# Performance work log

Measured on AMD Instinct MI355X. Metric: run time of the kernel, lower is better.

Reference implementation:

```python
import jax, jax.numpy as jnp
import numpy as np

EMBED_DIM = 1024
NUM_HEADS = 16
HEAD_DIM = EMBED_DIM // NUM_HEADS
LN_EPS = 1e-12
B, S = 2, 2048


def setup_inputs() -> dict:
    key = jax.random.key(0)
    ks = jax.random.split(key, 12)
    scale = 1.0 / np.sqrt(EMBED_DIM)
    d = EMBED_DIM
    return {
        "in_features": jax.random.normal(ks[0], (B, S, d), dtype=jnp.float32),
        "tgt_mask": jnp.ones((B, S), dtype=jnp.float32),
        "Wq": jax.random.normal(ks[1], (d, d), dtype=jnp.float32) * scale,
        "bq": jnp.zeros((d,), dtype=jnp.float32),
        "Wk": jax.random.normal(ks[2], (d, d), dtype=jnp.float32) * scale,
        "bk": jnp.zeros((d,), dtype=jnp.float32),
        "Wv": jax.random.normal(ks[3], (d, d), dtype=jnp.float32) * scale,
        "bv": jnp.zeros((d,), dtype=jnp.float32),
        "Wo": jax.random.normal(ks[4], (d, d), dtype=jnp.float32) * scale,
        "bo": jnp.zeros((d,), dtype=jnp.float32),
        "gamma": jnp.ones((d,), dtype=jnp.float32),
        "beta": jnp.zeros((d,), dtype=jnp.float32),
    }


def _split_heads(x):  # [B,S,D] -> [B,H,S,Dh]
    b, s, _ = x.shape
    return x.reshape(b, s, NUM_HEADS, HEAD_DIM).transpose(0, 2, 1, 3)


def reference(in_features, tgt_mask, Wq, bq, Wk, bk, Wv, bv, Wo, bo, gamma, beta):
    # Self-attention (tgt_features defaults to in_features). Dropout in eval mode (identity).
    q = _split_heads(in_features @ Wq.T + bq)
    k = _split_heads(in_features @ Wk.T + bk)
    v = _split_heads(in_features @ Wv.T + bv)
    # scores: [B,H,S,S]
    scores = jnp.einsum("bhqd,bhkd->bhqk", q, k) / jnp.sqrt(jnp.float32(HEAD_DIM))
    scores = scores + (1.0 - tgt_mask)[:, None, None, :] * (-100000.0)
    attn = jax.nn.softmax(scores, axis=-1)
    ctx = jnp.einsum("bhqk,bhkd->bhqd", attn, v)  # [B,H,S,Dh]
    ctx = ctx.transpose(0, 2, 1, 3).reshape(in_features.shape)  # merge heads
    out = ctx @ Wo.T + bo
    x = out + in_features
    mu = jnp.mean(x, axis=-1, keepdims=True)
    var = jnp.mean(jnp.square(x - mu), axis=-1, keepdims=True)
    return (x - mu) / jnp.sqrt(var + LN_EPS) * gamma + beta
```

## Files before the change

kernel.cpp:

```cpp
#include <hip/hip_runtime.h>
#include <hip/hip_bf16.h>

#define DM   1024
#define HEADS 16
#define DH    64
#define SEQ  2048
#define BATCH   2

typedef __attribute__((ext_vector_type(8))) short short8;
typedef __attribute__((ext_vector_type(4))) short bf16x4;
typedef __attribute__((ext_vector_type(4))) float floatx4;

__device__ __forceinline__ short f2b(float f) {
    union { float f; unsigned u; } v; v.f = f;
    unsigned r = v.u + 0x7FFFu + ((v.u >> 16) & 1u);
    return (short)(r >> 16);
}

__device__ __forceinline__ void async_copy16(const short* gsrc, short* ldst) {
    __builtin_amdgcn_global_load_lds(
        (const __attribute__((address_space(1))) void*)gsrc,
        (__attribute__((address_space(3))) void*)ldst,
        16, 0, 0);
}

__global__ __launch_bounds__(256) void cvt_all(const float* __restrict__ x,
        const float* __restrict__ wq, const float* __restrict__ wk,
        const float* __restrict__ wv, const float* __restrict__ wo,
        short* __restrict__ xb, short* __restrict__ wqkv, short* __restrict__ wob)
{
    const int b = blockIdx.x;
    const float* src; short* dst; int idx;
    if (b < 4096)      { src = x;  dst = xb;                idx = b; }
    else if (b < 5120) { src = wq; dst = wqkv;              idx = b - 4096; }
    else if (b < 6144) { src = wk; dst = wqkv + (1 << 20);  idx = b - 5120; }
    else if (b < 7168) { src = wv; dst = wqkv + (2 << 20);  idx = b - 6144; }
    else               { src = wo; dst = wob;               idx = b - 7168; }
    const int i = idx * 256 + threadIdx.x;
    floatx4 v = ((const floatx4*)src)[i];
    bf16x4 o;
    o.x = f2b(v.x); o.y = f2b(v.y); o.z = f2b(v.z); o.w = f2b(v.w);
    ((bf16x4*)dst)[i] = o;
}

__global__ __launch_bounds__(256) void gemm_qkv(const short* __restrict__ A,
        const short* __restrict__ B,
        const float* __restrict__ bq, const float* __restrict__ bk,
        const float* __restrict__ bv,
        short* __restrict__ qw, short* __restrict__ kw, short* __restrict__ vw)
{
    __shared__ short As[128 * 32];
    __shared__ short Bs[128 * 32];
    const int m0 = blockIdx.x * 128, n0 = blockIdx.y * 128;
    const int w = threadIdx.x >> 6, lane = threadIdx.x & 63;
    const int l16 = lane & 15, quad = lane >> 4;
    const int wm = w >> 1, wn = w & 1;
    const int lr = lane >> 2, lc = (lane & 3) * 8;

    floatx4 acc[4][4];
#pragma unroll
    for (int i = 0; i < 4; ++i)
#pragma unroll
        for (int j = 0; j < 4; ++j) acc[i][j] = (floatx4){0.f, 0.f, 0.f, 0.f};

    for (int kt = 0; kt < DM / 32; ++kt) {
        const int k0 = kt * 32;
        __syncthreads();
        async_copy16(A + (size_t)(m0 + w * 32 + lr) * DM + k0 + lc,      &As[w * 1024]);
        async_copy16(A + (size_t)(m0 + w * 32 + 16 + lr) * DM + k0 + lc, &As[w * 1024 + 512]);
        async_copy16(B + (size_t)(n0 + w * 32 + lr) * DM + k0 + lc,      &Bs[w * 1024]);
        async_copy16(B + (size_t)(n0 + w * 32 + 16 + lr) * DM + k0 + lc, &Bs[w * 1024 + 512]);
        __syncthreads();

        short8 af[4], bf[4];
#pragma unroll
        for (int i = 0; i < 4; ++i)
            af[i] = *(const short8*)&As[(wm * 64 + i * 16 + l16) * 32 + quad * 8];
#pragma unroll
        for (int j = 0; j < 4; ++j)
            bf[j] = *(const short8*)&Bs[(wn * 64 + j * 16 + l16) * 32 + quad * 8];
#pragma unroll
        for (int i = 0; i < 4; ++i)
#pragma unroll
            for (int j = 0; j < 4; ++j)
                acc[i][j] = __builtin_amdgcn_mfma_f32_16x16x32_bf16(af[i], bf[j], acc[i][j], 0, 0, 0);
    }

    const int m_base = m0 + wm * 64 + quad * 4;
#pragma unroll
    for (int j = 0; j < 4; ++j) {
        const int nb = n0 + wn * 64 + j * 16;
        const int t = nb >> 10;
        const int nn = (nb & 1023) + l16;
        const int h = nn >> 6, dh = nn & 63;
        const float* bias = (t == 0) ? bq : (t == 1) ? bk : bv;
        short* dst = (t == 0) ? qw : (t == 1) ? kw : vw;
        const float bvv = bias[nn];
#pragma unroll
        for (int i = 0; i < 4; ++i)
#pragma unroll
            for (int r = 0; r < 4; ++r) {
                const int m = m_base + i * 16 + r;
                const int b = m >> 11, s = m & (SEQ - 1);
                dst[(((size_t)(b * HEADS + h)) * SEQ + s) * DH + dh] = f2b(acc[i][j][r] + bvv);
            }
    }
}

__global__ __launch_bounds__(256) void transpose_v(const short* __restrict__ v,
                                                   short* __restrict__ vt)
{
    __shared__ short tl[64][72];
    const int st = blockIdx.x;
    const int bh = blockIdx.y;
    const int t = threadIdx.x;
    const int row = t >> 2, off = (t & 3) * 16;
    const short* vp = v + ((size_t)bh * SEQ + st * 64 + row) * DH + off;
    *(short8*)&tl[row][off]     = *(const short8*)vp;
    *(short8*)&tl[row][off + 8] = *(const short8*)(vp + 8);
    __syncthreads();
    short8 o0, o1;
#pragma unroll
    for (int j = 0; j < 8; ++j) { o0[j] = tl[off + j][row]; o1[j] = tl[off + 8 + j][row]; }
    short* op = vt + ((size_t)bh * DH + row) * SEQ + st * 64 + off;
    *(short8*)op = o0;
    *(short8*)(op + 8) = o1;
}

__global__ __launch_bounds__(256) void attn_kernel(const short* __restrict__ q,
        const short* __restrict__ k, const short* __restrict__ vt,
        const float* __restrict__ mask, short* __restrict__ ctx)
{
    const int qtile = blockIdx.x;
    const int bh    = blockIdx.y;
    const int bidx  = bh >> 4;
    const int wave = threadIdx.x >> 6, lane = threadIdx.x & 63;
    const int l16 = lane & 15, quad = lane >> 4;

    __shared__ short k_lds[64][72];
    __shared__ short v_lds[64][72];
    __shared__ short p_lds[4][16][72];
    __shared__ float madd_lds[SEQ];

    {
        const int t = threadIdx.x;
        const float* mrow = mask + (size_t)bidx * SEQ;
#pragma unroll
        for (int i = 0; i < 8; ++i) {
            const int idx = t * 8 + i;
            madd_lds[idx] = (1.f - mrow[idx]) * (-100000.f);
        }
    }

    const int qrow = qtile * 64 + wave * 16 + l16;
    const short* qbase = q + ((size_t)bh * SEQ + qrow) * DH;
    short8 b_q[2];
#pragma unroll
    for (int ks = 0; ks < 2; ++ks)
        b_q[ks] = *(const short8*)(qbase + ks * 32 + quad * 8);

    float m_own = -1e30f;
    floatx4 o[4];
    floatx4 l_acc = (floatx4){0.f, 0.f, 0.f, 0.f};
#pragma unroll
    for (int d = 0; d < 4; ++d) o[d] = (floatx4){0.f, 0.f, 0.f, 0.f};

    const float scale = 0.125f;
    short8 ones;
#pragma unroll
    for (int j = 0; j < 8; ++j) ones[j] = (short)0x3F80;

    for (int kt = 0; kt < SEQ / 64; ++kt) {
        __syncthreads();
        {
            const int t = threadIdx.x;
            const int row = t >> 2;
            const int off = (t & 3) * 16;
            const short* kp = k + ((size_t)bh * SEQ + kt * 64 + row) * DH + off;
            *(short8*)&k_lds[row][off]     = *(const short8*)kp;
            *(short8*)&k_lds[row][off + 8] = *(const short8*)(kp + 8);
            const short* vp = vt + ((size_t)bh * DH + row) * SEQ + kt * 64 + off;
            *(short8*)&v_lds[row][off]     = *(const short8*)vp;
            *(short8*)&v_lds[row][off + 8] = *(const short8*)(vp + 8);
        }
        __syncthreads();

        float sv[4][4];
#pragma unroll
        for (int nt = 0; nt < 4; ++nt) {
            floatx4 acc = (floatx4){0.f, 0.f, 0.f, 0.f};
#pragma unroll
            for (int ks = 0; ks < 2; ++ks) {
                short8 a = *(const short8*)&k_lds[nt * 16 + l16][ks * 32 + quad * 8];
                acc = __builtin_amdgcn_mfma_f32_16x16x32_bf16(a, b_q[ks], acc, 0, 0, 0);
            }
            const floatx4 md = *(const floatx4*)&madd_lds[kt * 64 + nt * 16 + quad * 4];
#pragma unroll
            for (int r = 0; r < 4; ++r) sv[nt][r] = acc[r] * scale + md[r];
        }

        float tm = sv[0][0];
#pragma unroll
        for (int nt = 0; nt < 4; ++nt)
#pragma unroll
            for (int r = 0; r < 4; ++r) tm = fmaxf(tm, sv[nt][r]);
        tm = fmaxf(tm, __shfl_xor(tm, 16));
        tm = fmaxf(tm, __shfl_xor(tm, 32));
        const float nm = fmaxf(m_own, tm);
        const float alpha = __expf(m_own - nm);
        m_own = nm;

#pragma unroll
        for (int nt = 0; nt < 4; ++nt) {
            const float p0 = __expf(sv[nt][0] - nm);
            const float p1 = __expf(sv[nt][1] - nm);
            const float p2 = __expf(sv[nt][2] - nm);
            const float p3 = __expf(sv[nt][3] - nm);
            union { __hip_bfloat162 h[2]; bf16x4 v; } u;
            u.h[0] = __float22bfloat162_rn(make_float2(p0, p1));
            u.h[1] = __float22bfloat162_rn(make_float2(p2, p3));
            *(bf16x4*)&p_lds[wave][l16][nt * 16 + quad * 4] = u.v;
        }

        float ab[4];
#pragma unroll
        for (int r = 0; r < 4; ++r)
            ab[r] = __shfl(alpha, (lane & 48) | (quad * 4 + r));
#pragma unroll
        for (int d = 0; d < 4; ++d)
#pragma unroll
            for (int r = 0; r < 4; ++r) o[d][r] *= ab[r];
#pragma unroll
        for (int r = 0; r < 4; ++r) l_acc[r] *= ab[r];

#pragma unroll
        for (int ks2 = 0; ks2 < 2; ++ks2) {
            short8 pf = *(const short8*)&p_lds[wave][l16][ks2 * 32 + quad * 8];
#pragma unroll
            for (int d = 0; d < 4; ++d) {
                short8 vf = *(const short8*)&v_lds[d * 16 + l16][ks2 * 32 + quad * 8];
                o[d] = __builtin_amdgcn_mfma_f32_16x16x32_bf16(pf, vf, o[d], 0, 0, 0);
            }
            l_acc = __builtin_amdgcn_mfma_f32_16x16x32_bf16(pf, ones, l_acc, 0, 0, 0);
        }
    }

    const int h = bh & 15, bb = bh >> 4;
    const int srow = qtile * 64 + wave * 16 + quad * 4;
    float rl[4];
#pragma unroll
    for (int r = 0; r < 4; ++r) rl[r] = 1.f / l_acc[r];
#pragma unroll
    for (int d = 0; d < 4; ++d) {
        const int dh = d * 16 + l16;
#pragma unroll
        for (int r = 0; r < 4; ++r) {
            const float val = o[d][r] * rl[r];
            ctx[((size_t)(bb * SEQ + srow + r)) * DM + h * 64 + dh] = f2b(val);
        }
    }
}

__global__ __launch_bounds__(256) void gemm_o(const short* __restrict__ A,
        const short* __restrict__ B, const float* __restrict__ bo,
        const float* __restrict__ xin, float* __restrict__ out)
{
    __shared__ short As[128 * 32];
    __shared__ short Bs[128 * 32];
    const int m0 = blockIdx.x * 128, n0 = blockIdx.y * 128;
    const int w = threadIdx.x >> 6, lane = threadIdx.x & 63;
    const int l16 = lane & 15, quad = lane >> 4;
    const int wm = w >> 1, wn = w & 1;
    const int lr = lane >> 2, lc = (lane & 3) * 8;

    floatx4 acc[4][4];
#pragma unroll
    for (int i = 0; i < 4; ++i)
#pragma unroll
        for (int j = 0; j < 4; ++j) acc[i][j] = (floatx4){0.f, 0.f, 0.f, 0.f};

    for (int kt = 0; kt < DM / 32; ++kt) {
        const int k0 = kt * 32;
        __syncthreads();
        async_copy16(A + (size_t)(m0 + w * 32 + lr) * DM + k0 + lc,      &As[w * 1024]);
        async_copy16(A + (size_t)(m0 + w * 32 + 16 + lr) * DM + k0 + lc, &As[w * 1024 + 512]);
        async_copy16(B + (size_t)(n0 + w * 32 + lr) * DM + k0 + lc,      &Bs[w * 1024]);
        async_copy16(B + (size_t)(n0 + w * 32 + 16 + lr) * DM + k0 + lc, &Bs[w * 1024 + 512]);
        __syncthreads();

        short8 af[4], bf[4];
#pragma unroll
        for (int i = 0; i < 4; ++i)
            af[i] = *(const short8*)&As[(wm * 64 + i * 16 + l16) * 32 + quad * 8];
#pragma unroll
        for (int j = 0; j < 4; ++j)
            bf[j] = *(const short8*)&Bs[(wn * 64 + j * 16 + l16) * 32 + quad * 8];
#pragma unroll
        for (int i = 0; i < 4; ++i)
#pragma unroll
            for (int j = 0; j < 4; ++j)
                acc[i][j] = __builtin_amdgcn_mfma_f32_16x16x32_bf16(af[i], bf[j], acc[i][j], 0, 0, 0);
    }

    const int m_base = m0 + wm * 64 + quad * 4;
#pragma unroll
    for (int j = 0; j < 4; ++j) {
        const int n = n0 + wn * 64 + j * 16 + l16;
        const float bvv = bo[n];
#pragma unroll
        for (int i = 0; i < 4; ++i)
#pragma unroll
            for (int r = 0; r < 4; ++r) {
                const int m = m_base + i * 16 + r;
                const size_t idx = (size_t)m * DM + n;
                out[idx] = acc[i][j][r] + bvv + xin[idx];
            }
    }
}

__global__ __launch_bounds__(256) void ln_kernel(float* __restrict__ y,
        const float* __restrict__ gamma, const float* __restrict__ beta)
{
    const int row = blockIdx.x;
    const int t = threadIdx.x;
    const int wave = t >> 6, lane = t & 63;
    const floatx4 v = ((const floatx4*)(y + (size_t)row * DM))[t];
    float s  = v.x + v.y + v.z + v.w;
    float q2 = v.x * v.x + v.y * v.y + v.z * v.z + v.w * v.w;
#pragma unroll
    for (int off = 1; off < 64; off <<= 1) {
        s  += __shfl_xor(s, off);
        q2 += __shfl_xor(q2, off);
    }
    __shared__ float rs[4], rq[4];
    if (lane == 0) { rs[wave] = s; rq[wave] = q2; }
    __syncthreads();
    const float S  = rs[0] + rs[1] + rs[2] + rs[3];
    const float Q2 = rq[0] + rq[1] + rq[2] + rq[3];
    const float mu = S * (1.f / DM);
    float var = Q2 * (1.f / DM) - mu * mu;
    var = fmaxf(var, 0.f);
    const float rstd = rsqrtf(var + 1e-12f);
    const floatx4 g = ((const floatx4*)gamma)[t];
    const floatx4 bt = ((const floatx4*)beta)[t];
    floatx4 o;
    o.x = (v.x - mu) * rstd * g.x + bt.x;
    o.y = (v.y - mu) * rstd * g.y + bt.y;
    o.z = (v.z - mu) * rstd * g.z + bt.z;
    o.w = (v.w - mu) * rstd * g.w + bt.w;
    ((floatx4*)(y + (size_t)row * DM))[t] = o;
}

extern "C" void kernel_launch(void* const* d_in, const int* in_sizes, int n_in,
                              void* d_out, int out_size, void* d_ws, size_t ws_size,
                              hipStream_t stream) {
    const float* x     = (const float*)d_in[0];
    const float* mask  = (const float*)d_in[1];
    const float* Wq    = (const float*)d_in[2];
    const float* bq    = (const float*)d_in[3];
    const float* Wk    = (const float*)d_in[4];
    const float* bk    = (const float*)d_in[5];
    const float* Wv    = (const float*)d_in[6];
    const float* bv    = (const float*)d_in[7];
    const float* Wo    = (const float*)d_in[8];
    const float* bo    = (const float*)d_in[9];
    const float* gamma = (const float*)d_in[10];
    const float* beta  = (const float*)d_in[11];
    float* out = (float*)d_out;

    const size_t NTOK = (size_t)BATCH * SEQ * DM;
    const size_t WSZ  = (size_t)DM * DM;
    short* xb   = (short*)d_ws;
    short* wqkv = xb + NTOK;
    short* wob  = wqkv + 3 * WSZ;
    short* qw   = wob + WSZ;
    short* kw   = qw + NTOK;
    short* vw   = kw + NTOK;
    short* vtw  = vw + NTOK;
    short* ctxw = vw;

    dim3 blk(256);
    cvt_all<<<dim3(8192), blk, 0, stream>>>(x, Wq, Wk, Wv, Wo, xb, wqkv, wob);
    gemm_qkv<<<dim3(32, 24), blk, 0, stream>>>(xb, wqkv, bq, bk, bv, qw, kw, vw);
    transpose_v<<<dim3(SEQ / 64, BATCH * HEADS), blk, 0, stream>>>(vw, vtw);
    attn_kernel<<<dim3(SEQ / 64, BATCH * HEADS), blk, 0, stream>>>(qw, kw, vtw, mask, ctxw);
    gemm_o<<<dim3(32, 8), blk, 0, stream>>>(ctxw, wob, bo, x, out);
    ln_kernel<<<BATCH * SEQ, blk, 0, stream>>>(out, gamma, beta);
}
```

Measured before the change: 245.8 us.

## Use async global-to-LDS loads with XOR swizzle and fold scale into Q

Attention K/V tiles now load straight into LDS through global_load_lds using an XOR-swizzled unpadded layout, and the P tile uses the same swizzle. This removes the register round trip and padding, and the swizzle is meant to avoid bank conflicts. The 1/sqrt(d) scale moves into the Q projection epilogue, the mask is used as the initial MFMA accumulator, and the rescale of the output accumulator is skipped when no row max rises. Rounding Q after scaling changes bf16 rounding slightly, and the skip adds a branch.

```diff
diff --git a/kernel.cpp b/kernel.cpp
--- a/kernel.cpp
+++ b/kernel.cpp
@@ -95,6 +95,7 @@
         const int h = nn >> 6, dh = nn & 63;
         const float* bias = (t == 0) ? bq : (t == 1) ? bk : bv;
         short* dst = (t == 0) ? qw : (t == 1) ? kw : vw;
+        const float mulf = (t == 0) ? 0.125f : 1.0f;
         const float bvv = bias[nn];
 #pragma unroll
         for (int i = 0; i < 4; ++i)
@@ -102,7 +103,8 @@
             for (int r = 0; r < 4; ++r) {
                 const int m = m_base + i * 16 + r;
                 const int b = m >> 11, s = m & (SEQ - 1);
-                dst[(((size_t)(b * HEADS + h)) * SEQ + s) * DH + dh] = f2b(acc[i][j][r] + bvv);
+                dst[(((size_t)(b * HEADS + h)) * SEQ + s) * DH + dh] =
+                    f2b((acc[i][j][r] + bvv) * mulf);
             }
     }
 }
@@ -136,10 +138,11 @@
     const int bidx  = bh >> 4;
     const int wave = threadIdx.x >> 6, lane = threadIdx.x & 63;
     const int l16 = lane & 15, quad = lane >> 4;
-
-    __shared__ short k_lds[64][72];
-    __shared__ short v_lds[64][72];
-    __shared__ short p_lds[4][16][72];
+    const int lx = l16 & 7;
+
+    __shared__ short k_lds[64 * 64];
+    __shared__ short v_lds[64 * 64];
+    __shared__ short p_lds[4][16 * 64];
     __shared__ float madd_lds[SEQ];
 
     {
@@ -165,38 +168,41 @@
 #pragma unroll
     for (int d = 0; d < 4; ++d) o[d] = (floatx4){0.f, 0.f, 0.f, 0.f};
 
-    const float scale = 0.125f;
     short8 ones;
 #pragma unroll
     for (int j = 0; j < 8; ++j) ones[j] = (short)0x3F80;
 
+    const short* kbase0 = k  + (size_t)bh * SEQ * DH;
+    const short* vbase0 = vt + (size_t)bh * DH * SEQ;
+
     for (int kt = 0; kt < SEQ / 64; ++kt) {
         __syncthreads();
         {
-            const int t = threadIdx.x;
-            const int row = t >> 2;
-            const int off = (t & 3) * 16;
-            const short* kp = k + ((size_t)bh * SEQ + kt * 64 + row) * DH + off;
-            *(short8*)&k_lds[row][off]     = *(const short8*)kp;
-            *(short8*)&k_lds[row][off + 8] = *(const short8*)(kp + 8);
-            const short* vp = vt + ((size_t)bh * DH + row) * SEQ + kt * 64 + off;
-            *(short8*)&v_lds[row][off]     = *(const short8*)vp;
-            *(short8*)&v_lds[row][off + 8] = *(const short8*)(vp + 8);
+            const short* kbase = kbase0 + (size_t)(kt * 64) * DH;
+            const short* vbase = vbase0 + kt * 64;
+#pragma unroll
+            for (int i = 0; i < 2; ++i) {
+                const int slot = i * 256 + wave * 64 + lane;
+                const int row = slot >> 3, c = slot & 7;
+                const int g = c ^ (row & 7);
+                async_copy16(kbase + row * DH  + g * 8, &k_lds[(i * 256 + wave * 64) * 8]);
+                async_copy16(vbase + (size_t)row * SEQ + g * 8, &v_lds[(i * 256 + wave * 64) * 8]);
+            }
         }
         __syncthreads();
 
         float sv[4][4];
 #pragma unroll
         for (int nt = 0; nt < 4; ++nt) {
-            floatx4 acc = (floatx4){0.f, 0.f, 0.f, 0.f};
+            floatx4 acc = *(const floatx4*)&madd_lds[kt * 64 + nt * 16 + quad * 4];
 #pragma unroll
             for (int ks = 0; ks < 2; ++ks) {
-                short8 a = *(const short8*)&k_lds[nt * 16 + l16][ks * 32 + quad * 8];
+                short8 a = *(const short8*)
+                    &k_lds[(nt * 16 + l16) * 64 + (((ks * 4 + quad) ^ lx) * 8)];
                 acc = __builtin_amdgcn_mfma_f32_16x16x32_bf16(a, b_q[ks], acc, 0, 0, 0);
             }
-            const floatx4 md = *(const floatx4*)&madd_lds[kt * 64 + nt * 16 + quad * 4];
-#pragma unroll
-            for (int r = 0; r < 4; ++r) sv[nt][r] = acc[r] * scale + md[r];
+#pragma unroll
+            for (int r = 0; r < 4; ++r) sv[nt][r] = acc[r];
         }
 
         float tm = sv[0][0];
@@ -206,9 +212,8 @@
             for (int r = 0; r < 4; ++r) tm = fmaxf(tm, sv[nt][r]);
         tm = fmaxf(tm, __shfl_xor(tm, 16));
         tm = fmaxf(tm, __shfl_xor(tm, 32));
+        const int upd = __any(tm > m_own);
         const float nm = fmaxf(m_own, tm);
-        const float alpha = __expf(m_own - nm);
-        m_own = nm;
 
 #pragma unroll
         for (int nt = 0; nt < 4; ++nt) {
@@ -219,26 +224,33 @@
             union { __hip_bfloat162 h[2]; bf16x4 v; } u;
             u.h[0] = __float22bfloat162_rn(make_float2(p0, p1));
             u.h[1] = __float22bfloat162_rn(make_float2(p2, p3));
-            *(bf16x4*)&p_lds[wave][l16][nt * 16 + quad * 4] = u.v;
-        }
-
-        float ab[4];
-#pragma unroll
-        for (int r = 0; r < 4; ++r)
-            ab[r] = __shfl(alpha, (lane & 48) | (quad * 4 + r));
-#pragma unroll
-        for (int d = 0; d < 4; ++d)
-#pragma unroll
-            for (int r = 0; r < 4; ++r) o[d][r] *= ab[r];
-#pragma unroll
-        for (int r = 0; r < 4; ++r) l_acc[r] *= ab[r];
+            *(bf16x4*)&p_lds[wave][l16 * 64 +
+                (((nt * 2 + (quad >> 1)) ^ lx) * 8) + (quad & 1) * 4] = u.v;
+        }
+
+        if (upd) {
+            const float alpha = __expf(m_own - nm);
+            float ab[4];
+#pragma unroll
+            for (int r = 0; r < 4; ++r)
+                ab[r] = __shfl(alpha, (lane & 48) | (quad * 4 + r));
+#pragma unroll
+            for (int d = 0; d < 4; ++d)
+#pragma unroll
+                for (int r = 0; r < 4; ++r) o[d][r] *= ab[r];
+#pragma unroll
+            for (int r = 0; r < 4; ++r) l_acc[r] *= ab[r];
+        }
+        m_own = nm;
 
 #pragma unroll
         for (int ks2 = 0; ks2 < 2; ++ks2) {
-            short8 pf = *(const short8*)&p_lds[wave][l16][ks2 * 32 + quad * 8];
+            short8 pf = *(const short8*)
+                &p_lds[wave][l16 * 64 + (((ks2 * 4 + quad) ^ lx) * 8)];
 #pragma unroll
             for (int d = 0; d < 4; ++d) {
-                short8 vf = *(const short8*)&v_lds[d * 16 + l16][ks2 * 32 + quad * 8];
+                short8 vf = *(const short8*)
+                    &v_lds[(d * 16 + l16) * 64 + (((ks2 * 4 + quad) ^ lx) * 8)];
                 o[d] = __builtin_amdgcn_mfma_f32_16x16x32_bf16(pf, vf, o[d], 0, 0, 0);
             }
             l_acc = __builtin_amdgcn_mfma_f32_16x16x32_bf16(pf, ones, l_acc, 0, 0, 0);
```

Result: faster. 232.1 us (-5.6%).
